# Kernel optimization log

Measured on AMD Instinct MI355X. Metric: run time of the kernel, lower is better.

Reference implementation:

```python
import jax, jax.numpy as jnp
import numpy as np

DIM = 1024
FACTOR = 32          # factor_size
SUB = 8              # sub_blocks = (dim // factor_size) // 4
RANK = 8
B, T = 48, 256


def hamilton(A_stack):
    # A_stack: (rank, 4, SUB, SUB) -> H: (rank, 4*SUB, 4*SUB)
    r, i, j, k = A_stack[:, 0], A_stack[:, 1], A_stack[:, 2], A_stack[:, 3]
    row0 = jnp.concatenate([r, -i, -j, -k], axis=2)
    row1 = jnp.concatenate([i,  r, -k,  j], axis=2)
    row2 = jnp.concatenate([j,  k,  r, -i], axis=2)
    row3 = jnp.concatenate([k, -j,  i,  r], axis=2)
    return jnp.concatenate([row0, row1, row2, row3], axis=1)


def setup_inputs() -> dict:
    key = jax.random.key(0)
    k1, k2, k3 = jax.random.split(key, 3)
    x = jax.random.normal(k1, (B, T, DIM), dtype=jnp.float32)
    A_stack = jax.random.normal(k2, (RANK, 4, SUB, SUB), dtype=jnp.float32)
    # factors_B: orthogonal-init then scaled by (rank_index)^-0.5; random normal
    # scaled similarly is numerically equivalent in structure for the reference.
    scales = (jnp.arange(1, RANK + 1, dtype=jnp.float32) ** -0.5)[:, None, None]
    B_stack = jax.random.normal(k3, (RANK, FACTOR, FACTOR), dtype=jnp.float32) * scales
    bias = jnp.zeros((DIM,), dtype=jnp.float32)
    return {"x": x, "A_stack": A_stack, "B_stack": B_stack, "bias": bias}


def reference(x, A_stack, B_stack, bias):
    Bb, Tt, D = x.shape
    x_flat = x.reshape(-1, 4 * SUB, FACTOR)           # (n, 32, 32)
    H = hamilton(A_stack)                              # (r, 32, 32)
    wave_mod = jnp.einsum('nsi,rji->rnsj', x_flat, B_stack)   # (r, n, 32, 32)
    wave_out = jnp.einsum('rnsj,rks->nkj', wave_mod, H)       # (n, 32, 32)
    return wave_out.reshape(Bb, Tt, D) + bias
```

## Files before the change

kernel.cpp:

```cpp
#include <hip/hip_runtime.h>
#include <hip/hip_bf16.h>
#include <stdint.h>

#define M_TOT 12288
#define K_DIM 1024
#define N_DIM 1024
#define NTILE 16

typedef __attribute__((ext_vector_type(8))) __bf16 bf16x8;
typedef __attribute__((ext_vector_type(4))) float  f32x4;

__global__ __launch_bounds__(256)
void make_w(const float* __restrict__ A4,
            const float* __restrict__ Bs,
            __bf16* __restrict__ W)
{
    int idx = blockIdx.x * 256 + threadIdx.x;
    int dout = idx >> 10;
    int din  = idx & 1023;
    int k = dout >> 5, j = dout & 31;
    int s = din  >> 5, i = din  & 31;
    int kb = k >> 3, k8 = k & 7;
    int sb = s >> 3, s8 = s & 7;

    const int   comp[4][4] = {{0,1,2,3},{1,0,3,2},{2,3,0,1},{3,2,1,0}};
    const float sgn [4][4] = {{1.f,-1.f,-1.f,-1.f},
                              {1.f, 1.f,-1.f, 1.f},
                              {1.f, 1.f, 1.f,-1.f},
                              {1.f,-1.f, 1.f, 1.f}};
    int   c  = comp[kb][sb];
    float sg = sgn [kb][sb];

    float acc = 0.f;
    #pragma unroll
    for (int r = 0; r < 8; ++r) {
        float h = A4[((r*4 + c)*8 + k8)*8 + s8];
        float b = Bs[(r*32 + j)*32 + i];
        acc += h * b;
    }
    W[idx] = (__bf16)(sg * acc);
}

__global__ __launch_bounds__(256)
void cvt_x(const float* __restrict__ X, __bf16* __restrict__ Xb)
{
    size_t t = (size_t)blockIdx.x * 256 + threadIdx.x;
    const float4* x4 = (const float4*)X;
    float4 a = x4[2*t + 0];
    float4 b = x4[2*t + 1];
    bf16x8 v;
    v[0] = (__bf16)a.x; v[1] = (__bf16)a.y; v[2] = (__bf16)a.z; v[3] = (__bf16)a.w;
    v[4] = (__bf16)b.x; v[5] = (__bf16)b.y; v[6] = (__bf16)b.z; v[7] = (__bf16)b.w;
    *(bf16x8*)&Xb[t * 8] = v;
}

__device__ __forceinline__ void gl_lds16(const void* g, void* l)
{
    __builtin_amdgcn_global_load_lds(
        (const __attribute__((address_space(1))) void*)g,
        (__attribute__((address_space(3))) void*)l,
        16, 0, 0);
}

#define PHASE_MFMA(MH, NH, BF)                                                  \
    __builtin_amdgcn_s_barrier();                                               \
    asm volatile("s_waitcnt lgkmcnt(0)" ::: "memory");                          \
    __builtin_amdgcn_sched_barrier(0);                                          \
    __builtin_amdgcn_s_setprio(1);                                              \
    _Pragma("unroll")                                                           \
    for (int mi = 0; mi < 4; ++mi) {                                            \
        _Pragma("unroll")                                                       \
        for (int ni = 0; ni < 2; ++ni) {                                        \
            acc[(MH)*4+mi][(NH)*2+ni] = __builtin_amdgcn_mfma_f32_16x16x32_bf16(\
                aF[mi][0], BF[ni][0], acc[(MH)*4+mi][(NH)*2+ni], 0, 0, 0);      \
            acc[(MH)*4+mi][(NH)*2+ni] = __builtin_amdgcn_mfma_f32_16x16x32_bf16(\
                aF[mi][1], BF[ni][1], acc[(MH)*4+mi][(NH)*2+ni], 0, 0, 0);      \
        }                                                                       \
    }                                                                           \
    __builtin_amdgcn_s_setprio(0);                                              \
    __builtin_amdgcn_s_barrier();

__global__ __launch_bounds__(512, 2)
void gemm8p(const __bf16* __restrict__ A,
            const __bf16* __restrict__ BT,
            const float*  __restrict__ bias,
            float* __restrict__ C)
{
    __shared__ __align__(16) char lds[131072];

    const int tid  = threadIdx.x;
    const int wave = tid >> 6;
    const int lane = tid & 63;

    int wg  = blockIdx.x;
    int swz = (wg & 7) * 24 + (wg >> 3);
    const int brow = (swz >> 2) * 256;
    const int bcol = (swz & 3)  * 256;

    const int mg = wave >> 2;
    const int ng = wave & 3;
    const int fr = lane & 15;
    const int kq = lane >> 4;

    f32x4 acc[8][4];
    #pragma unroll
    for (int i = 0; i < 8; ++i)
        #pragma unroll
        for (int j = 0; j < 4; ++j)
            acc[i][j] = (f32x4){0.f, 0.f, 0.f, 0.f};

    auto stageA = [&](int ta, int mh) {
        if (ta >= NTILE) return;
        char* region = lds + (ta & 1) * 65536 + mh * 16384;
        #pragma unroll
        for (int q = 0; q < 2; ++q) {
            int s    = q * 8192 + tid * 16;
            int rwh  = s >> 7;
            int colb = (s & 127) ^ ((rwh & 7) << 4);
            int absr = ((rwh >> 6) << 7) + mh * 64 + (rwh & 63);
            const char* src = (const char*)A +
                ((size_t)(brow + absr) * K_DIM + ta * 64) * 2 + colb;
            gl_lds16(src, region + q * 8192 + wave * 1024);
        }
    };
    auto stageB = [&](int ta, int nh) {
        if (ta >= NTILE) return;
        char* region = lds + (ta & 1) * 65536 + 32768 + nh * 16384;
        #pragma unroll
        for (int q = 0; q < 2; ++q) {
            int s    = q * 8192 + tid * 16;
            int rwh  = s >> 7;
            int colb = (s & 127) ^ ((rwh & 7) << 4);
            int absr = ((rwh >> 5) << 6) + nh * 32 + (rwh & 31);
            const char* src = (const char*)BT +
                ((size_t)(bcol + absr) * K_DIM + ta * 64) * 2 + colb;
            gl_lds16(src, region + q * 8192 + wave * 1024);
        }
    };

    bf16x8 aF[4][2], bF0[2][2], bF1[2][2];

    auto ldA = [&](int bufb, int mh) {
        const char* base = lds + bufb + mh * 16384;
        #pragma unroll
        for (int mi = 0; mi < 4; ++mi) {
            int rwh = mg * 64 + mi * 16 + fr;
            #pragma unroll
            for (int ks = 0; ks < 2; ++ks) {
                int col = (ks * 64 + kq * 16) ^ ((rwh & 7) << 4);
                aF[mi][ks] = *(const bf16x8*)(base + rwh * 128 + col);
            }
        }
    };
    auto ldB = [&](bf16x8 (&bF)[2][2], int bufb, int nh) {
        const char* base = lds + bufb + 32768 + nh * 16384;
        #pragma unroll
        for (int ni = 0; ni < 2; ++ni) {
            int rwh = ng * 32 + ni * 16 + fr;
            #pragma unroll
            for (int ks = 0; ks < 2; ++ks) {
                int col = (ks * 64 + kq * 16) ^ ((rwh & 7) << 4);
                bF[ni][ks] = *(const bf16x8*)(base + rwh * 128 + col);
            }
        }
    };

    stageA(0, 0); stageA(0, 1); stageB(0, 0); stageB(0, 1);
    stageA(1, 0); stageA(1, 1);
    asm volatile("s_waitcnt vmcnt(4)" ::: "memory");
    __builtin_amdgcn_s_barrier();

    for (int t = 0; t < NTILE; ++t) {
        const int bufb = (t & 1) * 65536;

        ldA(bufb, 0);
        ldB(bF0, bufb, 0);
        stageB(t + 1, 0);
        PHASE_MFMA(0, 0, bF0)

        ldB(bF1, bufb, 1);
        stageB(t + 1, 1);
        PHASE_MFMA(0, 1, bF1)

        ldA(bufb, 1);
        stageA(t + 2, 0);
        PHASE_MFMA(1, 1, bF1)

        stageA(t + 2, 1);
        __builtin_amdgcn_s_barrier();
        __builtin_amdgcn_s_setprio(1);
        #pragma unroll
        for (int mi = 0; mi < 4; ++mi) {
            #pragma unroll
            for (int ni = 0; ni < 2; ++ni) {
                acc[4+mi][ni] = __builtin_amdgcn_mfma_f32_16x16x32_bf16(
                    aF[mi][0], bF0[ni][0], acc[4+mi][ni], 0, 0, 0);
                acc[4+mi][ni] = __builtin_amdgcn_mfma_f32_16x16x32_bf16(
                    aF[mi][1], bF0[ni][1], acc[4+mi][ni], 0, 0, 0);
            }
        }
        __builtin_amdgcn_s_setprio(0);
        if (t < NTILE - 2) {
            asm volatile("s_waitcnt vmcnt(4)" ::: "memory");
        } else {
            asm volatile("s_waitcnt vmcnt(0)" ::: "memory");
        }
        __builtin_amdgcn_s_barrier();
    }

    #pragma unroll
    for (int mf = 0; mf < 8; ++mf) {
        int r0 = brow + mg * 128 + mf * 16 + kq * 4;
        #pragma unroll
        for (int nf = 0; nf < 4; ++nf) {
            int c0 = bcol + ng * 64 + nf * 16 + fr;
            float bv = bias[c0];
            #pragma unroll
            for (int j = 0; j < 4; ++j)
                C[(size_t)(r0 + j) * N_DIM + c0] = acc[mf][nf][j] + bv;
        }
    }
}

extern "C" void kernel_launch(void* const* d_in, const int* in_sizes, int n_in,
                              void* d_out, int out_size, void* d_ws, size_t ws_size,
                              hipStream_t stream)
{
    const float* x    = (const float*)d_in[0];
    const float* A4   = (const float*)d_in[1];
    const float* Bs   = (const float*)d_in[2];
    const float* bias = (const float*)d_in[3];
    float* out = (float*)d_out;

    __bf16* W  = (__bf16*)d_ws;
    __bf16* Xb = (__bf16*)((char*)d_ws + (size_t)(1<<21));

    make_w<<<4096, 256, 0, stream>>>(A4, Bs, W);
    cvt_x<<<(M_TOT * K_DIM / 8 + 255) / 256, 256, 0, stream>>>(x, Xb);

    gemm8p<<<192, 512, 0, stream>>>(Xb, W, bias, out);
}
```

Before: 133.5 us.

## Shrink GEMM M-tile to 192 rows so grid fills all CUs

```diff
diff --git a/kernel.cpp b/kernel.cpp
--- a/kernel.cpp
+++ b/kernel.cpp
@@ -6,6 +6,8 @@
 #define K_DIM 1024
 #define N_DIM 1024
 #define NTILE 16
+
+#define LDSBUF 57344
 
 typedef __attribute__((ext_vector_type(8))) __bf16 bf16x8;
 typedef __attribute__((ext_vector_type(4))) float  f32x4;
@@ -62,19 +64,19 @@
         16, 0, 0);
 }
 
-#define PHASE_MFMA(MH, NH, BF)                                                  \
+#define PHASE_MFMA(SUB, NH, BF)                                                 \
     __builtin_amdgcn_s_barrier();                                               \
     asm volatile("s_waitcnt lgkmcnt(0)" ::: "memory");                          \
     __builtin_amdgcn_sched_barrier(0);                                          \
     __builtin_amdgcn_s_setprio(1);                                              \
     _Pragma("unroll")                                                           \
-    for (int mi = 0; mi < 4; ++mi) {                                            \
+    for (int mi = 0; mi < 3; ++mi) {                                            \
         _Pragma("unroll")                                                       \
         for (int ni = 0; ni < 2; ++ni) {                                        \
-            acc[(MH)*4+mi][(NH)*2+ni] = __builtin_amdgcn_mfma_f32_16x16x32_bf16(\
-                aF[mi][0], BF[ni][0], acc[(MH)*4+mi][(NH)*2+ni], 0, 0, 0);      \
-            acc[(MH)*4+mi][(NH)*2+ni] = __builtin_amdgcn_mfma_f32_16x16x32_bf16(\
-                aF[mi][1], BF[ni][1], acc[(MH)*4+mi][(NH)*2+ni], 0, 0, 0);      \
+            acc[(SUB)*3+mi][(NH)*2+ni] = __builtin_amdgcn_mfma_f32_16x16x32_bf16(\
+                aF[mi][0], BF[ni][0], acc[(SUB)*3+mi][(NH)*2+ni], 0, 0, 0);     \
+            acc[(SUB)*3+mi][(NH)*2+ni] = __builtin_amdgcn_mfma_f32_16x16x32_bf16(\
+                aF[mi][1], BF[ni][1], acc[(SUB)*3+mi][(NH)*2+ni], 0, 0, 0);     \
         }                                                                       \
     }                                                                           \
     __builtin_amdgcn_s_setprio(0);                                              \
@@ -86,15 +88,15 @@
             const float*  __restrict__ bias,
             float* __restrict__ C)
 {
-    __shared__ __align__(16) char lds[131072];
+    __shared__ __align__(16) char lds[2 * LDSBUF];
 
     const int tid  = threadIdx.x;
     const int wave = tid >> 6;
     const int lane = tid & 63;
 
     int wg  = blockIdx.x;
-    int swz = (wg & 7) * 24 + (wg >> 3);
-    const int brow = (swz >> 2) * 256;
+    int swz = (wg & 7) * 32 + (wg >> 3);
+    const int brow = (swz >> 2) * 192;
     const int bcol = (swz & 3)  * 256;
 
     const int mg = wave >> 2;
@@ -102,30 +104,29 @@
     const int fr = lane & 15;
     const int kq = lane >> 4;
 
-    f32x4 acc[8][4];
+    f32x4 acc[6][4];
     #pragma unroll
-    for (int i = 0; i < 8; ++i)
+    for (int i = 0; i < 6; ++i)
         #pragma unroll
         for (int j = 0; j < 4; ++j)
             acc[i][j] = (f32x4){0.f, 0.f, 0.f, 0.f};
 
-    auto stageA = [&](int ta, int mh) {
+    auto stageA = [&](int ta) {
         if (ta >= NTILE) return;
-        char* region = lds + (ta & 1) * 65536 + mh * 16384;
-        #pragma unroll
-        for (int q = 0; q < 2; ++q) {
+        char* region = lds + (ta & 1) * LDSBUF;
+        #pragma unroll
+        for (int q = 0; q < 3; ++q) {
             int s    = q * 8192 + tid * 16;
             int rwh  = s >> 7;
             int colb = (s & 127) ^ ((rwh & 7) << 4);
-            int absr = ((rwh >> 6) << 7) + mh * 64 + (rwh & 63);
             const char* src = (const char*)A +
-                ((size_t)(brow + absr) * K_DIM + ta * 64) * 2 + colb;
+                ((size_t)(brow + rwh) * K_DIM + ta * 64) * 2 + colb;
             gl_lds16(src, region + q * 8192 + wave * 1024);
         }
     };
     auto stageB = [&](int ta, int nh) {
         if (ta >= NTILE) return;
-        char* region = lds + (ta & 1) * 65536 + 32768 + nh * 16384;
+        char* region = lds + (ta & 1) * LDSBUF + 24576 + nh * 16384;
         #pragma unroll
         for (int q = 0; q < 2; ++q) {
             int s    = q * 8192 + tid * 16;
@@ -138,13 +139,13 @@
         }
     };
 
-    bf16x8 aF[4][2], bF0[2][2], bF1[2][2];
-
-    auto ldA = [&](int bufb, int mh) {
-        const char* base = lds + bufb + mh * 16384;
-        #pragma unroll
-        for (int mi = 0; mi < 4; ++mi) {
-            int rwh = mg * 64 + mi * 16 + fr;
+    bf16x8 aF[3][2], bF0[2][2], bF1[2][2];
+
+    auto ldA = [&](int bufb, int sub) {
+        const char* base = lds + bufb;
+        #pragma unroll
+        for (int mi = 0; mi < 3; ++mi) {
+            int rwh = mg * 96 + sub * 48 + mi * 16 + fr;
             #pragma unroll
             for (int ks = 0; ks < 2; ++ks) {
                 int col = (ks * 64 + kq * 16) ^ ((rwh & 7) << 4);
@@ -153,7 +154,7 @@
         }
     };
     auto ldB = [&](bf16x8 (&bF)[2][2], int bufb, int nh) {
-        const char* base = lds + bufb + 32768 + nh * 16384;
+        const char* base = lds + bufb + 24576 + nh * 16384;
         #pragma unroll
         for (int ni = 0; ni < 2; ++ni) {
             int rwh = ng * 32 + ni * 16 + fr;
@@ -165,13 +166,13 @@
         }
     };
 
-    stageA(0, 0); stageA(0, 1); stageB(0, 0); stageB(0, 1);
-    stageA(1, 0); stageA(1, 1);
-    asm volatile("s_waitcnt vmcnt(4)" ::: "memory");
+    stageA(0); stageB(0, 0); stageB(0, 1);
+    stageA(1);
+    asm volatile("s_waitcnt vmcnt(3)" ::: "memory");
     __builtin_amdgcn_s_barrier();
 
     for (int t = 0; t < NTILE; ++t) {
-        const int bufb = (t & 1) * 65536;
+        const int bufb = (t & 1) * LDSBUF;
 
         ldA(bufb, 0);
         ldB(bF0, bufb, 0);
@@ -183,25 +184,24 @@
         PHASE_MFMA(0, 1, bF1)
 
         ldA(bufb, 1);
-        stageA(t + 2, 0);
         PHASE_MFMA(1, 1, bF1)
 
-        stageA(t + 2, 1);
+        stageA(t + 2);
         __builtin_amdgcn_s_barrier();
         __builtin_amdgcn_s_setprio(1);
         #pragma unroll
-        for (int mi = 0; mi < 4; ++mi) {
+        for (int mi = 0; mi < 3; ++mi) {
             #pragma unroll
             for (int ni = 0; ni < 2; ++ni) {
-                acc[4+mi][ni] = __builtin_amdgcn_mfma_f32_16x16x32_bf16(
-                    aF[mi][0], bF0[ni][0], acc[4+mi][ni], 0, 0, 0);
-                acc[4+mi][ni] = __builtin_amdgcn_mfma_f32_16x16x32_bf16(
-                    aF[mi][1], bF0[ni][1], acc[4+mi][ni], 0, 0, 0);
+                acc[3+mi][ni] = __builtin_amdgcn_mfma_f32_16x16x32_bf16(
+                    aF[mi][0], bF0[ni][0], acc[3+mi][ni], 0, 0, 0);
+                acc[3+mi][ni] = __builtin_amdgcn_mfma_f32_16x16x32_bf16(
+                    aF[mi][1], bF0[ni][1], acc[3+mi][ni], 0, 0, 0);
             }
         }
         __builtin_amdgcn_s_setprio(0);
         if (t < NTILE - 2) {
-            asm volatile("s_waitcnt vmcnt(4)" ::: "memory");
+            asm volatile("s_waitcnt vmcnt(3)" ::: "memory");
         } else {
             asm volatile("s_waitcnt vmcnt(0)" ::: "memory");
         }
@@ -209,8 +209,8 @@
     }
 
     #pragma unroll
-    for (int mf = 0; mf < 8; ++mf) {
-        int r0 = brow + mg * 128 + mf * 16 + kq * 4;
+    for (int mf = 0; mf < 6; ++mf) {
+        int r0 = brow + mg * 96 + mf * 16 + kq * 4;
         #pragma unroll
         for (int nf = 0; nf < 4; ++nf) {
             int c0 = bcol + ng * 64 + nf * 16 + fr;
@@ -238,5 +238,5 @@
     make_w<<<4096, 256, 0, stream>>>(A4, Bs, W);
     cvt_x<<<(M_TOT * K_DIM / 8 + 255) / 256, 256, 0, stream>>>(x, Xb);
 
-    gemm8p<<<192, 512, 0, stream>>>(Xb, W, bias, out);
-}
+    gemm8p<<<256, 512, 0, stream>>>(Xb, W, bias, out);
+}
```

Result: faster. 129.7 us (-2.8%).
